# Kernel tuning notes

Measured on AMD Instinct MI355X. Metric: run time of the kernel, lower is better.

The kernel has to match this reference:

```python
import jax, jax.numpy as jnp
import numpy as np

B, T, IN, H, C = 256, 128, 64, 512, 11


def setup_inputs() -> dict:
    key = jax.random.key(0)
    ks = jax.random.split(key, 10)
    sc = 1.0 / np.sqrt(H).astype(np.float32)
    def w(k, shape, s):
        return jax.random.normal(k, shape, dtype=jnp.float32) * s
    return {
        "x": jax.random.normal(ks[0], (B, T, IN), dtype=jnp.float32),
        "t": jax.random.uniform(ks[1], (B, T), dtype=jnp.float32),
        # nn.LSTMCell params (gate order i, f, g, o)
        "W_ih": w(ks[2], (4 * H, IN), sc),
        "W_hh": w(ks[3], (4 * H, H), sc),
        "b_ih": jnp.zeros((4 * H,), jnp.float32),
        "b_hh": jnp.zeros((4 * H,), jnp.float32),
        # f_node: Linear(H,H) -> Tanh -> Linear(H,H)
        "W1": w(ks[4], (H, H), sc),
        "b1": jnp.zeros((H,), jnp.float32),
        "W2": w(ks[5], (H, H), sc),
        "b2": jnp.zeros((H,), jnp.float32),
        # ODELSTM per-step output Linear(H, out_feature=H)
        "Wo": w(ks[6], (H, H), sc),
        "bo": jnp.zeros((H,), jnp.float32),
        # model head Linear(H, num_classes)
        "Wc": w(ks[7], (C, H), sc),
        "bc": jnp.zeros((C,), jnp.float32),
    }


def reference(x, t, W_ih, W_hh, b_ih, b_hh, W1, b1, W2, b2, Wo, bo, Wc, bc):
    def f_node(y):  # [B,H] -> [B,H]
        return jnp.tanh(y @ W1.T + b1) @ W2.T + b2

    def rk4(y, dt):  # dt: [B,1]
        k1 = f_node(y)
        k2 = f_node(y + k1 * dt * 0.5)
        k3 = f_node(y + k2 * dt * 0.5)
        k4 = f_node(y + k3 * dt)
        return y + dt * (k1 + 2.0 * k2 + 2.0 * k3 + k4) / 6.0

    def step(carry, inp):
        h, c = carry
        xt, ts = inp  # [B,IN], [B]
        z = xt @ W_ih.T + h @ W_hh.T + (b_ih + b_hh)
        i, f, g, o = jnp.split(z, 4, axis=-1)
        c = jax.nn.sigmoid(f) * c + jax.nn.sigmoid(i) * jnp.tanh(g)
        h = jax.nn.sigmoid(o) * jnp.tanh(c)
        dt = (ts * (1.0 / 3.0))[:, None]  # 3 fixed unfolds per timestep
        for _ in range(3):
            h = rk4(h, dt)
        out = h @ Wo.T + bo  # ODELSTM per-step output projection
        return (h, c), out

    h0 = jnp.zeros((x.shape[0], W_hh.shape[1]), x.dtype)
    (_h, _c), outs = jax.lax.scan(
        step, (h0, h0), (jnp.swapaxes(x, 0, 1), jnp.swapaxes(t, 0, 1))
    )
    outs = jnp.swapaxes(outs, 0, 1)  # [B,T,H]
    return outs @ Wc.T + bc  # [B,T,num_classes]
```

## Files before the change

kernel.cpp:

```cpp
#include <hip/hip_runtime.h>
#include <stdint.h>


#define H_  512
#define B_  256
#define T_  128
#define IN_ 64
#define NC_ 11
#define LD_ 520
#define FSTRIDE 64

typedef _Float16 h8v __attribute__((ext_vector_type(8)));
typedef float    f4v __attribute__((ext_vector_type(4)));
typedef unsigned long long ull;

__device__ __forceinline__ float fsigm(float x) { return 1.0f / (1.0f + __expf(-x)); }
__device__ __forceinline__ float ftanh(float x) { return 1.0f - 2.0f / (1.0f + __expf(2.0f * x)); }


__global__ void prep_M(const float* __restrict__ W1, const float* __restrict__ W2,
                       float* __restrict__ Mtmp) {
  __shared__ float w1s[8][512];
  int tid = threadIdx.x;
  int n0 = blockIdx.x * 8;
  for (int i = tid; i < 8 * 512; i += 256) {
    int nn = i >> 9, m = i & 511;
    w1s[nn][m] = W1[(n0 + nn) * 512 + m];
  }
  __syncthreads();
  float acc0[8] = {0,0,0,0,0,0,0,0}, acc1[8] = {0,0,0,0,0,0,0,0};
  for (int m = 0; m < 512; ++m) {
    float a = W2[m * 512 + tid];
    float b = W2[m * 512 + 256 + tid];
#pragma unroll
    for (int j = 0; j < 8; ++j) { acc0[j] += a * w1s[j][m]; acc1[j] += b * w1s[j][m]; }
  }
  for (int j = 0; j < 8; ++j) {
    Mtmp[(size_t)tid * 512 + n0 + j]         = acc0[j];
    Mtmp[(size_t)(tid + 256) * 512 + n0 + j] = acc1[j];
  }
}

__global__ void prep_small(const float* __restrict__ W1, const float* __restrict__ b2,
                           const float* __restrict__ Wc, const float* __restrict__ Wo,
                           const float* __restrict__ bo, const float* __restrict__ bc,
                           float* __restrict__ dvec, float* __restrict__ Wco,
                           float* __restrict__ bprime) {
  __shared__ float wcs[NC_ * 512];
  int tid = threadIdx.x;
  if (blockIdx.x == 0) {
    for (int n = tid; n < 512; n += 256) {
      float acc = 0.f;
      for (int m = 0; m < 512; ++m) acc += b2[m] * W1[n * 512 + m];
      dvec[n] = acc;
    }
  } else if (blockIdx.x == 1) {
    if (tid < NC_) {
      float acc = bc[tid];
      for (int m = 0; m < 512; ++m) acc += Wc[tid * 512 + m] * bo[m];
      bprime[tid] = acc;
    }
  } else {
    for (int i = tid; i < NC_ * 512; i += 256) wcs[i] = Wc[i];
    __syncthreads();
    int h = (blockIdx.x - 2) * 256 + tid;
    float acc[NC_];
#pragma unroll
    for (int c = 0; c < NC_; ++c) acc[c] = 0.f;
    for (int m = 0; m < 512; ++m) {
      float wo = Wo[m * 512 + h];
#pragma unroll
      for (int c = 0; c < NC_; ++c) acc[c] += wo * wcs[c * 512 + m];
    }
    for (int c = 0; c < NC_; ++c) Wco[c * 512 + h] = acc[c];
  }
}

__global__ void prep_wtilde(const float* __restrict__ Whh, const float* __restrict__ Wih,
                            _Float16* __restrict__ Wtil) {
  int gidx = blockIdx.x * 256 + threadIdx.x;
  int lane = gidx & 63, fb = gidx >> 6;
  int kc = fb % 18; int t2 = fb / 18;
  int t = t2 & 31, g = t2 >> 5;
  int n = g * 512 + t * 16 + (lane & 15);
  int k = kc * 32 + ((lane >> 4) & 3) * 8;
  _Float16 vals[8];
  if (k < 512) {
#pragma unroll
    for (int j = 0; j < 8; ++j) vals[j] = (_Float16)Whh[(size_t)n * 512 + k + j];
  } else {
#pragma unroll
    for (int j = 0; j < 8; ++j) vals[j] = (_Float16)Wih[(size_t)n * 64 + (k - 512) + j];
  }
  *(h8v*)(Wtil + (size_t)fb * 512 + lane * 8) = *(h8v*)vals;
}

__global__ void prep_fragW(const float* __restrict__ W, _Float16* __restrict__ dst) {
  int gidx = blockIdx.x * 256 + threadIdx.x;
  int lane = gidx & 63, fb = gidx >> 6;
  int t = fb >> 4, kc = fb & 15;
  int n = t * 16 + (lane & 15);
  int k = kc * 32 + ((lane >> 4) & 3) * 8;
  _Float16 vals[8];
#pragma unroll
  for (int j = 0; j < 8; ++j) vals[j] = (_Float16)W[(size_t)n * 512 + k + j];
  *(h8v*)(dst + (size_t)fb * 512 + lane * 8) = *(h8v*)vals;
}

__global__ void prep_fragM(const float* __restrict__ Mtmp, _Float16* __restrict__ dst) {
  int gidx = blockIdx.x * 256 + threadIdx.x;
  int lane = gidx & 63, fb = gidx >> 6;
  int t = fb >> 4, kc = fb & 15;
  int n = t * 16 + (lane & 15);
  int k = kc * 32 + ((lane >> 4) & 3) * 8;
  _Float16 vals[8];
#pragma unroll
  for (int j = 0; j < 8; ++j) vals[j] = (_Float16)Mtmp[(size_t)(k + j) * 512 + n];
  *(h8v*)(dst + (size_t)fb * 512 + lane * 8) = *(h8v*)vals;
}


__device__ __forceinline__ void phase_exchange(int* __restrict__ flagsC,
                                               ull* __restrict__ Xb,
                                               _Float16* __restrict__ ACT,
                                               int s, int phase) {
  const int tid = threadIdx.x;
  __syncthreads();
  {
    int m = tid >> 4, ch = tid & 15;
    ull v = *(const ull*)(ACT + m * LD_ + s * 64 + ch * 4);
    __hip_atomic_store(Xb + m * 128 + s * 16 + ch, v,
                       __ATOMIC_RELAXED, __HIP_MEMORY_SCOPE_AGENT);
  }
  __builtin_amdgcn_s_waitcnt(0);
  __syncthreads();
  if (tid == 0)
    __hip_atomic_store(flagsC + s * FSTRIDE, phase,
                       __ATOMIC_RELAXED, __HIP_MEMORY_SCOPE_AGENT);
  {
    const int* fp = flagsC + (tid & 7) * FSTRIDE;
    for (;;) {
      int f = __hip_atomic_load(fp, __ATOMIC_RELAXED, __HIP_MEMORY_SCOPE_AGENT);
      if (__all(f >= phase)) break;
      __builtin_amdgcn_s_sleep(1);
    }
  }
  __asm__ volatile("" ::: "memory");
  ull tv[8];
#pragma unroll
  for (int i = 0; i < 8; ++i) {
    int idx = i * 256 + tid;
    int os = idx >> 8, r = idx & 255, m = r >> 4, ch = r & 15;
    tv[i] = __hip_atomic_load(Xb + m * 128 + os * 16 + ch,
                              __ATOMIC_RELAXED, __HIP_MEMORY_SCOPE_AGENT);
  }
#pragma unroll
  for (int i = 0; i < 8; ++i) {
    int idx = i * 256 + tid;
    int os = idx >> 8, r = idx & 255, m = r >> 4, ch = r & 15;
    *(ull*)(ACT + m * LD_ + os * 64 + ch * 4) = tv[i];
  }
  __syncthreads();
}


__device__ __forceinline__ f4v mm_lds(const _Float16* __restrict__ ACT,
                                      const _Float16* __restrict__ Ws,
                                      int w, int lane) {
  f4v e = {0,0,0,0}, o = {0,0,0,0};
  const _Float16* arow = ACT + (lane & 15) * LD_ + (lane >> 4) * 8;
  const h8v* b = (const h8v*)Ws;
#pragma unroll
  for (int kc = 0; kc < 16; kc += 2) {
    e = __builtin_amdgcn_mfma_f32_16x16x32_f16(*(const h8v*)(arow + kc * 32),
                                               b[(w * 16 + kc) * 64 + lane], e, 0, 0, 0);
    o = __builtin_amdgcn_mfma_f32_16x16x32_f16(*(const h8v*)(arow + (kc + 1) * 32),
                                               b[(w * 16 + kc + 1) * 64 + lane], o, 0, 0, 0);
  }
  return e + o;
}

__device__ __forceinline__ f4v mm_reg(const _Float16* __restrict__ ACT,
                                      const h8v* __restrict__ mreg, int lane) {
  f4v e = {0,0,0,0}, o = {0,0,0,0};
  const _Float16* arow = ACT + (lane & 15) * LD_ + (lane >> 4) * 8;
#pragma unroll
  for (int kc = 0; kc < 16; kc += 2) {
    e = __builtin_amdgcn_mfma_f32_16x16x32_f16(*(const h8v*)(arow + kc * 32),
                                               mreg[kc], e, 0, 0, 0);
    o = __builtin_amdgcn_mfma_f32_16x16x32_f16(*(const h8v*)(arow + (kc + 1) * 32),
                                               mreg[kc + 1], o, 0, 0, 0);
  }
  return e + o;
}


__launch_bounds__(256, 1)
__global__ void recur(const float* __restrict__ x,
                      const float* __restrict__ tin,
                      const float* __restrict__ bih,
                      const float* __restrict__ bhh,
                      const float* __restrict__ b1g,
                      const float* __restrict__ b2g,
                      const _Float16* __restrict__ Wtil,
                      const _Float16* __restrict__ W1T,
                      const _Float16* __restrict__ W2T,
                      const _Float16* __restrict__ MF,
                      const float* __restrict__ dvec,
                      _Float16* __restrict__ Hsave,
                      ull* __restrict__ Xchg,
                      int* __restrict__ flags) {
  const int blk = blockIdx.x, c = blk & 15, s = blk >> 4;
  const int tid = threadIdx.x, w = tid >> 6, lane = tid & 63;
  const int lm = lane & 15, quad = lane >> 4;
  const int col = s * 64 + w * 16 + lm;

  __shared__ __align__(16) _Float16 W1s[4 * 16 * 512];
  __shared__ __align__(16) _Float16 W2s[4 * 16 * 512];
  __shared__ __align__(16) _Float16 ACT[16 * LD_];

  {
    const h8v* g1 = (const h8v*)(W1T + (size_t)s * 32768);
    const h8v* g2 = (const h8v*)(W2T + (size_t)s * 32768);
    h8v* l1 = (h8v*)W1s; h8v* l2 = (h8v*)W2s;
    for (int i = tid; i < 4096; i += 256) { l1[i] = g1[i]; l2[i] = g2[i]; }
  }
  h8v mreg[16];
  {
    const h8v* gm = (const h8v*)(MF + ((size_t)(4 * s + w) * 16) * 512);
#pragma unroll
    for (int kc = 0; kc < 16; ++kc) mreg[kc] = gm[kc * 64 + lane];
  }
  for (int i = tid; i < 16 * LD_; i += 256) ACT[i] = (_Float16)0.f;

  const float zb0 = bih[col] + bhh[col];
  const float zb1 = bih[512 + col] + bhh[512 + col];
  const float zb2 = bih[1024 + col] + bhh[1024 + col];
  const float zb3 = bih[1536 + col] + bhh[1536 + col];
  const float b1r = b1g[col], dvr = dvec[col], b2r = b2g[col];

  float c_[4] = {0,0,0,0}, h_[4] = {0,0,0,0};
  float u1a[4], SSa[4], SMa[4];
  int phase = 0;
  int* flagsC = flags + c * 512;
  __syncthreads();

  for (int ts = 0; ts < T_; ++ts) {
    float dt_[4];
#pragma unroll
    for (int r = 0; r < 4; ++r)
      dt_[r] = tin[(c * 16 + quad * 4 + r) * T_ + ts] * (1.0f / 3.0f);

    {
      f4v z0 = {0,0,0,0}, z1 = {0,0,0,0}, z2 = {0,0,0,0}, z3 = {0,0,0,0};
      const _Float16* arow = ACT + lm * LD_ + quad * 8;
      const h8v* wt = (const h8v*)Wtil;
      const int tb = 4 * s + w;
#pragma unroll
      for (int kc = 0; kc < 16; ++kc) {
        h8v av = *(const h8v*)(arow + kc * 32);
        z0 = __builtin_amdgcn_mfma_f32_16x16x32_f16(av, wt[(size_t)((0 * 32 + tb) * 18 + kc) * 64 + lane], z0, 0, 0, 0);
        z1 = __builtin_amdgcn_mfma_f32_16x16x32_f16(av, wt[(size_t)((1 * 32 + tb) * 18 + kc) * 64 + lane], z1, 0, 0, 0);
        z2 = __builtin_amdgcn_mfma_f32_16x16x32_f16(av, wt[(size_t)((2 * 32 + tb) * 18 + kc) * 64 + lane], z2, 0, 0, 0);
        z3 = __builtin_amdgcn_mfma_f32_16x16x32_f16(av, wt[(size_t)((3 * 32 + tb) * 18 + kc) * 64 + lane], z3, 0, 0, 0);
      }
      const float* xr = x + ((size_t)(c * 16 + lm) * T_ + ts) * IN_ + quad * 8;
#pragma unroll
      for (int kx = 0; kx < 2; ++kx) {
        float4 f0 = *(const float4*)(xr + kx * 32);
        float4 f1 = *(const float4*)(xr + kx * 32 + 4);
        h8v av;
        av[0] = (_Float16)f0.x; av[1] = (_Float16)f0.y; av[2] = (_Float16)f0.z; av[3] = (_Float16)f0.w;
        av[4] = (_Float16)f1.x; av[5] = (_Float16)f1.y; av[6] = (_Float16)f1.z; av[7] = (_Float16)f1.w;
        int kc = 16 + kx;
        z0 = __builtin_amdgcn_mfma_f32_16x16x32_f16(av, wt[(size_t)((0 * 32 + tb) * 18 + kc) * 64 + lane], z0, 0, 0, 0);
        z1 = __builtin_amdgcn_mfma_f32_16x16x32_f16(av, wt[(size_t)((1 * 32 + tb) * 18 + kc) * 64 + lane], z1, 0, 0, 0);
        z2 = __builtin_amdgcn_mfma_f32_16x16x32_f16(av, wt[(size_t)((2 * 32 + tb) * 18 + kc) * 64 + lane], z2, 0, 0, 0);
        z3 = __builtin_amdgcn_mfma_f32_16x16x32_f16(av, wt[(size_t)((3 * 32 + tb) * 18 + kc) * 64 + lane], z3, 0, 0, 0);
      }
      __syncthreads();
#pragma unroll
      for (int r = 0; r < 4; ++r) {
        float zi = z0[r] + zb0, zf = z1[r] + zb1, zg = z2[r] + zb2, zo = z3[r] + zb3;
        float cv = fsigm(zf) * c_[r] + fsigm(zi) * ftanh(zg);
        c_[r] = cv;
        h_[r] = fsigm(zo) * ftanh(cv);
        ACT[(quad * 4 + r) * LD_ + col] = (_Float16)h_[r];
      }
    }
    ++phase;
    phase_exchange(flagsC, Xchg + (size_t)((phase & 1) * 16 + c) * 2048, ACT, s, phase);

    {
      f4v D = mm_lds(ACT, W1s, w, lane);
      __syncthreads();
#pragma unroll
      for (int r = 0; r < 4; ++r) {
        float uv = D[r] + b1r;
        u1a[r] = uv;
        float t1v = ftanh(uv);
        SSa[r] = t1v;
        ACT[(quad * 4 + r) * LD_ + col] = (_Float16)t1v;
      }
    }
    ++phase;
    phase_exchange(flagsC, Xchg + (size_t)((phase & 1) * 16 + c) * 2048, ACT, s, phase);

#pragma unroll 1
    for (int uf = 0; uf < 3; ++uf) {
      {
        f4v D = mm_reg(ACT, mreg, lane);
        __syncthreads();
#pragma unroll
        for (int r = 0; r < 4; ++r) {
          float Dv = D[r];
          float u2 = u1a[r] + 0.5f * dt_[r] * (Dv + dvr);
          SMa[r] = Dv;
          float t2v = ftanh(u2);
          SSa[r] += 2.0f * t2v;
          ACT[(quad * 4 + r) * LD_ + col] = (_Float16)t2v;
        }
      }
      ++phase;
      phase_exchange(flagsC, Xchg + (size_t)((phase & 1) * 16 + c) * 2048, ACT, s, phase);

      {
        f4v D = mm_reg(ACT, mreg, lane);
        __syncthreads();
#pragma unroll
        for (int r = 0; r < 4; ++r) {
          float Dv = D[r];
          float u3 = u1a[r] + 0.5f * dt_[r] * (Dv + dvr);
          SMa[r] += 2.0f * Dv;
          float t3v = ftanh(u3);
          SSa[r] += 2.0f * t3v;
          ACT[(quad * 4 + r) * LD_ + col] = (_Float16)t3v;
        }
      }
      ++phase;
      phase_exchange(flagsC, Xchg + (size_t)((phase & 1) * 16 + c) * 2048, ACT, s, phase);

      {
        f4v D = mm_reg(ACT, mreg, lane);
        __syncthreads();
#pragma unroll
        for (int r = 0; r < 4; ++r) {
          float Dv = D[r];
          float u4 = u1a[r] + dt_[r] * (Dv + dvr);
          SMa[r] += 2.0f * Dv;
          float t4v = ftanh(u4);
          SSa[r] += t4v;
          ACT[(quad * 4 + r) * LD_ + col] = (uf < 2) ? (_Float16)t4v : (_Float16)SSa[r];
        }
      }
      ++phase;
      phase_exchange(flagsC, Xchg + (size_t)((phase & 1) * 16 + c) * 2048, ACT, s, phase);

      if (uf < 2) {
        f4v D = mm_reg(ACT, mreg, lane);
        __syncthreads();
#pragma unroll
        for (int r = 0; r < 4; ++r) {
          float Dv = D[r];
          SMa[r] += Dv;
          float un = u1a[r] + (dt_[r] * (1.0f / 6.0f)) * SMa[r] + dt_[r] * dvr;
          u1a[r] = un;
          float t1v = ftanh(un);
          SSa[r] += t1v;
          ACT[(quad * 4 + r) * LD_ + col] = (_Float16)t1v;
        }
        ++phase;
        phase_exchange(flagsC, Xchg + (size_t)((phase & 1) * 16 + c) * 2048, ACT, s, phase);
      }
    }

    {
      f4v D = mm_lds(ACT, W2s, w, lane);
      __syncthreads();
#pragma unroll
      for (int r = 0; r < 4; ++r) {
        h_[r] += (dt_[r] * (1.0f / 6.0f)) * D[r] + (3.0f * dt_[r]) * b2r;
        _Float16 hv = (_Float16)h_[r];
        ACT[(quad * 4 + r) * LD_ + col] = hv;
        Hsave[((size_t)(ts + 1) * B_ + c * 16 + quad * 4 + r) * H_ + col] = hv;
      }
    }
    ++phase;
    phase_exchange(flagsC, Xchg + (size_t)((phase & 1) * 16 + c) * 2048, ACT, s, phase);
  }
}

__global__ void final_out(const _Float16* __restrict__ Hsave,
                          const float* __restrict__ Wco,
                          const float* __restrict__ bprime,
                          float* __restrict__ out) {
  __shared__ float wcs[NC_][520];
  int tid = threadIdx.x;
  for (int i = tid; i < NC_ * 512; i += 256) wcs[i >> 9][i & 511] = Wco[i];
  __syncthreads();
  int r0 = blockIdx.x * 64;
  int rl = tid >> 4, cc = tid & 15;
  for (int pass = 0; pass < 4; ++pass) {
    int row = r0 + pass * 16 + rl;
    int b = row >> 7, t = row & 127;
    const _Float16* hrow = Hsave + ((size_t)(t + 1) * B_ + b) * H_;
    if (cc < NC_) {
      float acc = 0.f;
      for (int k8 = 0; k8 < 64; ++k8) {
        h8v hv = *(const h8v*)(hrow + k8 * 8);
#pragma unroll
        for (int j = 0; j < 8; ++j) acc += (float)hv[j] * wcs[cc][k8 * 8 + j];
      }
      out[(size_t)row * NC_ + cc] = acc + bprime[cc];
    }
  }
}

extern "C" void kernel_launch(void* const* d_in, const int* in_sizes, int n_in,
                              void* d_out, int out_size, void* d_ws, size_t ws_size,
                              hipStream_t stream) {
  (void)in_sizes; (void)n_in; (void)out_size; (void)ws_size;
  const float* x   = (const float*)d_in[0];
  const float* tin = (const float*)d_in[1];
  const float* Wih = (const float*)d_in[2];
  const float* Whh = (const float*)d_in[3];
  const float* bih = (const float*)d_in[4];
  const float* bhh = (const float*)d_in[5];
  const float* W1  = (const float*)d_in[6];
  const float* b1  = (const float*)d_in[7];
  const float* W2  = (const float*)d_in[8];
  const float* b2  = (const float*)d_in[9];
  const float* Wo  = (const float*)d_in[10];
  const float* bo  = (const float*)d_in[11];
  const float* Wc  = (const float*)d_in[12];
  const float* bc  = (const float*)d_in[13];

  char* ws = (char*)d_ws;
  size_t off = 0;
  auto alloc = [&](size_t bytes) -> void* {
    void* p = ws + off;
    off = (off + bytes + 1023) & ~(size_t)1023;
    return p;
  };
  _Float16* Wtil  = (_Float16*)alloc((size_t)2304 * 512 * 2);
  _Float16* W1T   = (_Float16*)alloc((size_t)512 * 512 * 2);
  _Float16* W2T   = (_Float16*)alloc((size_t)512 * 512 * 2);
  _Float16* MF    = (_Float16*)alloc((size_t)512 * 512 * 2);
  float*    Mtmp  = (float*)alloc((size_t)512 * 512 * 4);
  float*    dvec  = (float*)alloc(512 * 4);
  float*    WcoF  = (float*)alloc((size_t)NC_ * 512 * 4);
  float*    bprim = (float*)alloc(64);
  _Float16* Hsave = (_Float16*)alloc((size_t)(T_ + 1) * B_ * H_ * 2);
  ull*      Xchg  = (ull*)alloc((size_t)2 * 16 * 2048 * 8);
  int*      flags = (int*)alloc(16 * 512 * 4);

  hipMemsetAsync(flags, 0, 16 * 512 * 4, stream);

  prep_M<<<64, 256, 0, stream>>>(W1, W2, Mtmp);
  prep_small<<<4, 256, 0, stream>>>(W1, b2, Wc, Wo, bo, bc, dvec, WcoF, bprim);
  prep_wtilde<<<576, 256, 0, stream>>>(Whh, Wih, Wtil);
  prep_fragW<<<128, 256, 0, stream>>>(W1, W1T);
  prep_fragW<<<128, 256, 0, stream>>>(W2, W2T);
  prep_fragM<<<128, 256, 0, stream>>>(Mtmp, MF);
  recur<<<128, 256, 0, stream>>>(x, tin, bih, bhh, b1, b2, Wtil, W1T, W2T, MF,
                                 dvec, Hsave, Xchg, flags);
  final_out<<<512, 256, 0, stream>>>(Hsave, WcoF, bprim, (float*)d_out);
}
```

Measured before the change: 4.645 ms.

## Publish activations per-wave directly and use per-wave flags in phase exchange

Each wave now writes its four fp16 results straight from registers to the global exchange buffer in a column-major layout and raises its own per-wave flag, instead of staging through LDS and synchronizing the whole block twice before one thread sets a per-block flag. Readers poll 32 per-wave flags and scatter the gathered data back into the row-major LDS activation tile with transposing stores. This removes two block barriers and an LDS round-trip per phase. In exchange there is more flag polling traffic and strided 2-byte LDS stores that may bank-conflict.

```diff
diff --git a/kernel.cpp b/kernel.cpp
--- a/kernel.cpp
+++ b/kernel.cpp
@@ -11,6 +11,7 @@
 #define FSTRIDE 64
 
 typedef _Float16 h8v __attribute__((ext_vector_type(8)));
+typedef _Float16 h4v __attribute__((ext_vector_type(4)));
 typedef float    f4v __attribute__((ext_vector_type(4)));
 typedef unsigned long long ull;
 
@@ -121,24 +122,16 @@
 
 
 __device__ __forceinline__ void phase_exchange(int* __restrict__ flagsC,
-                                               ull* __restrict__ Xb,
+                                               const ull* __restrict__ Xb,
                                                _Float16* __restrict__ ACT,
-                                               int s, int phase) {
+                                               int s, int w, int lane, int phase) {
   const int tid = threadIdx.x;
-  __syncthreads();
-  {
-    int m = tid >> 4, ch = tid & 15;
-    ull v = *(const ull*)(ACT + m * LD_ + s * 64 + ch * 4);
-    __hip_atomic_store(Xb + m * 128 + s * 16 + ch, v,
-                       __ATOMIC_RELAXED, __HIP_MEMORY_SCOPE_AGENT);
-  }
   __builtin_amdgcn_s_waitcnt(0);
-  __syncthreads();
-  if (tid == 0)
-    __hip_atomic_store(flagsC + s * FSTRIDE, phase,
+  if (lane == 0)
+    __hip_atomic_store(flagsC + (s * 4 + w) * FSTRIDE, phase,
                        __ATOMIC_RELAXED, __HIP_MEMORY_SCOPE_AGENT);
   {
-    const int* fp = flagsC + (tid & 7) * FSTRIDE;
+    const int* fp = flagsC + (lane & 31) * FSTRIDE;
     for (;;) {
       int f = __hip_atomic_load(fp, __ATOMIC_RELAXED, __HIP_MEMORY_SCOPE_AGENT);
       if (__all(f >= phase)) break;
@@ -148,17 +141,17 @@
   __asm__ volatile("" ::: "memory");
   ull tv[8];
 #pragma unroll
-  for (int i = 0; i < 8; ++i) {
-    int idx = i * 256 + tid;
-    int os = idx >> 8, r = idx & 255, m = r >> 4, ch = r & 15;
-    tv[i] = __hip_atomic_load(Xb + m * 128 + os * 16 + ch,
-                              __ATOMIC_RELAXED, __HIP_MEMORY_SCOPE_AGENT);
-  }
-#pragma unroll
-  for (int i = 0; i < 8; ++i) {
-    int idx = i * 256 + tid;
-    int os = idx >> 8, r = idx & 255, m = r >> 4, ch = r & 15;
-    *(ull*)(ACT + m * LD_ + os * 64 + ch * 4) = tv[i];
+  for (int os = 0; os < 8; ++os)
+    tv[os] = __hip_atomic_load(Xb + os * 256 + tid,
+                               __ATOMIC_RELAXED, __HIP_MEMORY_SCOPE_AGENT);
+  {
+    const int colq = tid >> 2, q4 = (tid & 3) * 4;
+#pragma unroll
+    for (int os = 0; os < 8; ++os) {
+      h4v v = __builtin_bit_cast(h4v, tv[os]);
+      _Float16* dst = ACT + q4 * LD_ + os * 64 + colq;
+      dst[0] = v[0]; dst[LD_] = v[1]; dst[2 * LD_] = v[2]; dst[3 * LD_] = v[3];
+    }
   }
   __syncthreads();
 }
@@ -242,8 +235,12 @@
   float c_[4] = {0,0,0,0}, h_[4] = {0,0,0,0};
   float u1a[4], SSa[4], SMa[4];
   int phase = 0;
-  int* flagsC = flags + c * 512;
+  int* flagsC = flags + c * 32 * FSTRIDE;
+  const size_t pubi = (size_t)col * 4 + quad;
   __syncthreads();
+
+#define PUBLISH(pv) __hip_atomic_store(Xb + pubi, __builtin_bit_cast(ull, pv), \
+                                       __ATOMIC_RELAXED, __HIP_MEMORY_SCOPE_AGENT)
 
   for (int ts = 0; ts < T_; ++ts) {
     float dt_[4];
@@ -278,39 +275,45 @@
         z2 = __builtin_amdgcn_mfma_f32_16x16x32_f16(av, wt[(size_t)((2 * 32 + tb) * 18 + kc) * 64 + lane], z2, 0, 0, 0);
         z3 = __builtin_amdgcn_mfma_f32_16x16x32_f16(av, wt[(size_t)((3 * 32 + tb) * 18 + kc) * 64 + lane], z3, 0, 0, 0);
       }
-      __syncthreads();
+      ++phase;
+      ull* Xb = Xchg + (size_t)((phase & 1) * 16 + c) * 2048;
+      h4v pv;
 #pragma unroll
       for (int r = 0; r < 4; ++r) {
         float zi = z0[r] + zb0, zf = z1[r] + zb1, zg = z2[r] + zb2, zo = z3[r] + zb3;
         float cv = fsigm(zf) * c_[r] + fsigm(zi) * ftanh(zg);
         c_[r] = cv;
         h_[r] = fsigm(zo) * ftanh(cv);
-        ACT[(quad * 4 + r) * LD_ + col] = (_Float16)h_[r];
-      }
-    }
-    ++phase;
-    phase_exchange(flagsC, Xchg + (size_t)((phase & 1) * 16 + c) * 2048, ACT, s, phase);
+        pv[r] = (_Float16)h_[r];
+      }
+      PUBLISH(pv);
+      phase_exchange(flagsC, Xb, ACT, s, w, lane, phase);
+    }
 
     {
       f4v D = mm_lds(ACT, W1s, w, lane);
-      __syncthreads();
+      ++phase;
+      ull* Xb = Xchg + (size_t)((phase & 1) * 16 + c) * 2048;
+      h4v pv;
 #pragma unroll
       for (int r = 0; r < 4; ++r) {
         float uv = D[r] + b1r;
         u1a[r] = uv;
         float t1v = ftanh(uv);
         SSa[r] = t1v;
-        ACT[(quad * 4 + r) * LD_ + col] = (_Float16)t1v;
-      }
-    }
-    ++phase;
-    phase_exchange(flagsC, Xchg + (size_t)((phase & 1) * 16 + c) * 2048, ACT, s, phase);
+        pv[r] = (_Float16)t1v;
+      }
+      PUBLISH(pv);
+      phase_exchange(flagsC, Xb, ACT, s, w, lane, phase);
+    }
 
 #pragma unroll 1
     for (int uf = 0; uf < 3; ++uf) {
       {
         f4v D = mm_reg(ACT, mreg, lane);
-        __syncthreads();
+        ++phase;
+        ull* Xb = Xchg + (size_t)((phase & 1) * 16 + c) * 2048;
+        h4v pv;
 #pragma unroll
         for (int r = 0; r < 4; ++r) {
           float Dv = D[r];
@@ -318,15 +321,17 @@
           SMa[r] = Dv;
           float t2v = ftanh(u2);
           SSa[r] += 2.0f * t2v;
-          ACT[(quad * 4 + r) * LD_ + col] = (_Float16)t2v;
+          pv[r] = (_Float16)t2v;
         }
-      }
-      ++phase;
-      phase_exchange(flagsC, Xchg + (size_t)((phase & 1) * 16 + c) * 2048, ACT, s, phase);
+        PUBLISH(pv);
+        phase_exchange(flagsC, Xb, ACT, s, w, lane, phase);
+      }
 
       {
         f4v D = mm_reg(ACT, mreg, lane);
-        __syncthreads();
+        ++phase;
+        ull* Xb = Xchg + (size_t)((phase & 1) * 16 + c) * 2048;
+        h4v pv;
 #pragma unroll
         for (int r = 0; r < 4; ++r) {
           float Dv = D[r];
@@ -334,15 +339,17 @@
           SMa[r] += 2.0f * Dv;
           float t3v = ftanh(u3);
           SSa[r] += 2.0f * t3v;
-          ACT[(quad * 4 + r) * LD_ + col] = (_Float16)t3v;
+          pv[r] = (_Float16)t3v;
         }
-      }
-      ++phase;
-      phase_exchange(flagsC, Xchg + (size_t)((phase & 1) * 16 + c) * 2048, ACT, s, phase);
+        PUBLISH(pv);
+        phase_exchange(flagsC, Xb, ACT, s, w, lane, phase);
+      }
 
       {
         f4v D = mm_reg(ACT, mreg, lane);
-        __syncthreads();
+        ++phase;
+        ull* Xb = Xchg + (size_t)((phase & 1) * 16 + c) * 2048;
+        h4v pv;
 #pragma unroll
         for (int r = 0; r < 4; ++r) {
           float Dv = D[r];
@@ -350,15 +357,17 @@
           SMa[r] += 2.0f * Dv;
           float t4v = ftanh(u4);
           SSa[r] += t4v;
-          ACT[(quad * 4 + r) * LD_ + col] = (uf < 2) ? (_Float16)t4v : (_Float16)SSa[r];
+          pv[r] = (uf < 2) ? (_Float16)t4v : (_Float16)SSa[r];
         }
-      }
-      ++phase;
-      phase_exchange(flagsC, Xchg + (size_t)((phase & 1) * 16 + c) * 2048, ACT, s, phase);
+        PUBLISH(pv);
+        phase_exchange(flagsC, Xb, ACT, s, w, lane, phase);
+      }
 
       if (uf < 2) {
         f4v D = mm_reg(ACT, mreg, lane);
-        __syncthreads();
+        ++phase;
+        ull* Xb = Xchg + (size_t)((phase & 1) * 16 + c) * 2048;
+        h4v pv;
 #pragma unroll
         for (int r = 0; r < 4; ++r) {
           float Dv = D[r];
@@ -367,27 +376,30 @@
           u1a[r] = un;
           float t1v = ftanh(un);
           SSa[r] += t1v;
-          ACT[(quad * 4 + r) * LD_ + col] = (_Float16)t1v;
+          pv[r] = (_Float16)t1v;
         }
-        ++phase;
-        phase_exchange(flagsC, Xchg + (size_t)((phase & 1) * 16 + c) * 2048, ACT, s, phase);
+        PUBLISH(pv);
+        phase_exchange(flagsC, Xb, ACT, s, w, lane, phase);
       }
     }
 
     {
       f4v D = mm_lds(ACT, W2s, w, lane);
-      __syncthreads();
+      ++phase;
+      ull* Xb = Xchg + (size_t)((phase & 1) * 16 + c) * 2048;
+      h4v pv;
 #pragma unroll
       for (int r = 0; r < 4; ++r) {
         h_[r] += (dt_[r] * (1.0f / 6.0f)) * D[r] + (3.0f * dt_[r]) * b2r;
         _Float16 hv = (_Float16)h_[r];
-        ACT[(quad * 4 + r) * LD_ + col] = hv;
+        pv[r] = hv;
         Hsave[((size_t)(ts + 1) * B_ + c * 16 + quad * 4 + r) * H_ + col] = hv;
       }
-    }
-    ++phase;
-    phase_exchange(flagsC, Xchg + (size_t)((phase & 1) * 16 + c) * 2048, ACT, s, phase);
-  }
+      PUBLISH(pv);
+      phase_exchange(flagsC, Xb, ACT, s, w, lane, phase);
+    }
+  }
+#undef PUBLISH
 }
 
 __global__ void final_out(const _Float16* __restrict__ Hsave,
@@ -452,9 +464,9 @@
   float*    bprim = (float*)alloc(64);
   _Float16* Hsave = (_Float16*)alloc((size_t)(T_ + 1) * B_ * H_ * 2);
   ull*      Xchg  = (ull*)alloc((size_t)2 * 16 * 2048 * 8);
-  int*      flags = (int*)alloc(16 * 512 * 4);
-
-  hipMemsetAsync(flags, 0, 16 * 512 * 4, stream);
+  int*      flags = (int*)alloc(16 * 32 * FSTRIDE * 4);
+
+  hipMemsetAsync(flags, 0, 16 * 32 * FSTRIDE * 4, stream);
 
   prep_M<<<64, 256, 0, stream>>>(W1, W2, Mtmp);
   prep_small<<<4, 256, 0, stream>>>(W1, b2, Wc, Wo, bo, bc, dvec, WcoF, bprim);
```

After: 5.920 ms. 27.5% more time.

## Replace flag-based block barrier with epoch-tagged data exchange

Applied to the files above, without the earlier changes.

Each exchanged value now carries its phase number in the upper 32 bits of a 64-bit word. Consumers poll the data slots directly until every tag reaches the current phase, which removes the separate flag stores, the waitcnt, and two of the __syncthreads per exchange, and threads publish straight from registers instead of staging through LDS. The cost is that each exchanged word holds half as much fp16 payload, so exchange traffic doubles, and every thread spins on several remote loads.

```diff
diff --git a/kernel.cpp b/kernel.cpp
--- a/kernel.cpp
+++ b/kernel.cpp
@@ -8,11 +8,11 @@
 #define IN_ 64
 #define NC_ 11
 #define LD_ 520
-#define FSTRIDE 64
 
 typedef _Float16 h8v __attribute__((ext_vector_type(8)));
 typedef float    f4v __attribute__((ext_vector_type(4)));
 typedef unsigned long long ull;
+typedef unsigned int uint;
 
 __device__ __forceinline__ float fsigm(float x) { return 1.0f / (1.0f + __expf(-x)); }
 __device__ __forceinline__ float ftanh(float x) { return 1.0f - 2.0f / (1.0f + __expf(2.0f * x)); }
@@ -120,47 +120,66 @@
 }
 
 
-__device__ __forceinline__ void phase_exchange(int* __restrict__ flagsC,
-                                               ull* __restrict__ Xb,
+__device__ __forceinline__ ull pack2(_Float16 d0, _Float16 d1, int ep) {
+  uint lo = (uint)__builtin_bit_cast(unsigned short, d0) |
+            ((uint)__builtin_bit_cast(unsigned short, d1) << 16);
+  return (ull)lo | ((ull)(uint)ep << 32);
+}
+
+__device__ __forceinline__ void publish2(ull* __restrict__ XbA, ull* __restrict__ XbB,
+                                         int slot, const float* pv, int phase) {
+  ull eA = pack2((_Float16)pv[0], (_Float16)pv[1], phase);
+  ull eB = pack2((_Float16)pv[2], (_Float16)pv[3], phase);
+  __hip_atomic_store(XbA + slot, eA, __ATOMIC_RELAXED, __HIP_MEMORY_SCOPE_AGENT);
+  __hip_atomic_store(XbB + slot, eB, __ATOMIC_RELAXED, __HIP_MEMORY_SCOPE_AGENT);
+}
+
+__device__ __forceinline__ void store_tile(_Float16* __restrict__ ACT, int q, int cg,
+                                           const ull* a, const ull* b) {
+  uint l0 = (uint)a[0], l1 = (uint)a[1], l2 = (uint)a[2], l3 = (uint)a[3];
+  uint m0 = (uint)b[0], m1 = (uint)b[1], m2 = (uint)b[2], m3 = (uint)b[3];
+  ull r0 = (ull)((l0 & 0xffffu) | (l1 << 16)) | ((ull)((l2 & 0xffffu) | (l3 << 16)) << 32);
+  ull r1 = (ull)((l0 >> 16) | (l1 & 0xffff0000u)) | ((ull)((l2 >> 16) | (l3 & 0xffff0000u)) << 32);
+  ull r2 = (ull)((m0 & 0xffffu) | (m1 << 16)) | ((ull)((m2 & 0xffffu) | (m3 << 16)) << 32);
+  ull r3 = (ull)((m0 >> 16) | (m1 & 0xffff0000u)) | ((ull)((m2 >> 16) | (m3 & 0xffff0000u)) << 32);
+  _Float16* dst = ACT + (q * 4) * LD_ + cg * 4;
+  *(ull*)(dst)           = r0;
+  *(ull*)(dst + LD_)     = r1;
+  *(ull*)(dst + 2 * LD_) = r2;
+  *(ull*)(dst + 3 * LD_) = r3;
+}
+
+__device__ __forceinline__ void gather_restage(const ull* __restrict__ XbA,
+                                               const ull* __restrict__ XbB,
                                                _Float16* __restrict__ ACT,
-                                               int s, int phase) {
+                                               int s, int lane, int phase) {
   const int tid = threadIdx.x;
-  __syncthreads();
-  {
-    int m = tid >> 4, ch = tid & 15;
-    ull v = *(const ull*)(ACT + m * LD_ + s * 64 + ch * 4);
-    __hip_atomic_store(Xb + m * 128 + s * 16 + ch, v,
-                       __ATOMIC_RELAXED, __HIP_MEMORY_SCOPE_AGENT);
-  }
-  __builtin_amdgcn_s_waitcnt(0);
-  __syncthreads();
-  if (tid == 0)
-    __hip_atomic_store(flagsC + s * FSTRIDE, phase,
-                       __ATOMIC_RELAXED, __HIP_MEMORY_SCOPE_AGENT);
-  {
-    const int* fp = flagsC + (tid & 7) * FSTRIDE;
-    for (;;) {
-      int f = __hip_atomic_load(fp, __ATOMIC_RELAXED, __HIP_MEMORY_SCOPE_AGENT);
-      if (__all(f >= phase)) break;
-      __builtin_amdgcn_s_sleep(1);
-    }
-  }
-  __asm__ volatile("" ::: "memory");
-  ull tv[8];
-#pragma unroll
-  for (int i = 0; i < 8; ++i) {
-    int idx = i * 256 + tid;
-    int os = idx >> 8, r = idx & 255, m = r >> 4, ch = r & 15;
-    tv[i] = __hip_atomic_load(Xb + m * 128 + os * 16 + ch,
-                              __ATOMIC_RELAXED, __HIP_MEMORY_SCOPE_AGENT);
-  }
-#pragma unroll
-  for (int i = 0; i < 8; ++i) {
-    int idx = i * 256 + tid;
-    int os = idx >> 8, r = idx & 255, m = r >> 4, ch = r & 15;
-    *(ull*)(ACT + m * LD_ + os * 64 + ch * 4) = tv[i];
-  }
-  __syncthreads();
+  const int q0 = tid >> 7, cg = tid & 127;
+  const int base0 = q0 * 512 + cg * 4;
+  const int base1 = (q0 + 2) * 512 + cg * 4;
+  const int gslot = s * 64 + (lane & 3) * 16;
+  const uint p = (uint)phase;
+  ull a0[4], b0[4], a1[4], b1[4];
+  for (;;) {
+    ull g = __hip_atomic_load(XbA + gslot, __ATOMIC_RELAXED, __HIP_MEMORY_SCOPE_AGENT);
+#pragma unroll
+    for (int j = 0; j < 4; ++j) {
+      a0[j] = __hip_atomic_load(XbA + base0 + j, __ATOMIC_RELAXED, __HIP_MEMORY_SCOPE_AGENT);
+      b0[j] = __hip_atomic_load(XbB + base0 + j, __ATOMIC_RELAXED, __HIP_MEMORY_SCOPE_AGENT);
+      a1[j] = __hip_atomic_load(XbA + base1 + j, __ATOMIC_RELAXED, __HIP_MEMORY_SCOPE_AGENT);
+      b1[j] = __hip_atomic_load(XbB + base1 + j, __ATOMIC_RELAXED, __HIP_MEMORY_SCOPE_AGENT);
+    }
+    bool ok = ((uint)(g >> 32) >= p);
+#pragma unroll
+    for (int j = 0; j < 4; ++j) {
+      ok = ok && ((uint)(a0[j] >> 32) >= p) && ((uint)(b0[j] >> 32) >= p) &&
+                 ((uint)(a1[j] >> 32) >= p) && ((uint)(b1[j] >> 32) >= p);
+    }
+    if (__all(ok)) break;
+    __builtin_amdgcn_s_sleep(1);
+  }
+  store_tile(ACT, q0, cg, a0, b0);
+  store_tile(ACT, q0 + 2, cg, a1, b1);
 }
 
 
@@ -208,8 +227,7 @@
                       const _Float16* __restrict__ MF,
                       const float* __restrict__ dvec,
                       _Float16* __restrict__ Hsave,
-                      ull* __restrict__ Xchg,
-                      int* __restrict__ flags) {
+                      ull* __restrict__ Xchg) {
   const int blk = blockIdx.x, c = blk & 15, s = blk >> 4;
   const int tid = threadIdx.x, w = tid >> 6, lane = tid & 63;
   const int lm = lane & 15, quad = lane >> 4;
@@ -242,8 +260,11 @@
   float c_[4] = {0,0,0,0}, h_[4] = {0,0,0,0};
   float u1a[4], SSa[4], SMa[4];
   int phase = 0;
-  int* flagsC = flags + c * 512;
+  const int slotq = quad * 512 + col;
   __syncthreads();
+
+#define XSEL() ull* XbA = Xchg + (size_t)(((phase & 1) * 16 + c) * 2) * 2048; \
+               ull* XbB = XbA + 2048
 
   for (int ts = 0; ts < T_; ++ts) {
     float dt_[4];
@@ -278,39 +299,47 @@
         z2 = __builtin_amdgcn_mfma_f32_16x16x32_f16(av, wt[(size_t)((2 * 32 + tb) * 18 + kc) * 64 + lane], z2, 0, 0, 0);
         z3 = __builtin_amdgcn_mfma_f32_16x16x32_f16(av, wt[(size_t)((3 * 32 + tb) * 18 + kc) * 64 + lane], z3, 0, 0, 0);
       }
-      __syncthreads();
+      ++phase;
+      XSEL();
+      float pv[4];
 #pragma unroll
       for (int r = 0; r < 4; ++r) {
         float zi = z0[r] + zb0, zf = z1[r] + zb1, zg = z2[r] + zb2, zo = z3[r] + zb3;
         float cv = fsigm(zf) * c_[r] + fsigm(zi) * ftanh(zg);
         c_[r] = cv;
         h_[r] = fsigm(zo) * ftanh(cv);
-        ACT[(quad * 4 + r) * LD_ + col] = (_Float16)h_[r];
-      }
-    }
-    ++phase;
-    phase_exchange(flagsC, Xchg + (size_t)((phase & 1) * 16 + c) * 2048, ACT, s, phase);
+        pv[r] = h_[r];
+      }
+      publish2(XbA, XbB, slotq, pv, phase);
+      gather_restage(XbA, XbB, ACT, s, lane, phase);
+      __syncthreads();
+    }
 
     {
       f4v D = mm_lds(ACT, W1s, w, lane);
-      __syncthreads();
+      ++phase;
+      XSEL();
+      float pv[4];
 #pragma unroll
       for (int r = 0; r < 4; ++r) {
         float uv = D[r] + b1r;
         u1a[r] = uv;
         float t1v = ftanh(uv);
         SSa[r] = t1v;
-        ACT[(quad * 4 + r) * LD_ + col] = (_Float16)t1v;
-      }
-    }
-    ++phase;
-    phase_exchange(flagsC, Xchg + (size_t)((phase & 1) * 16 + c) * 2048, ACT, s, phase);
+        pv[r] = t1v;
+      }
+      publish2(XbA, XbB, slotq, pv, phase);
+      gather_restage(XbA, XbB, ACT, s, lane, phase);
+      __syncthreads();
+    }
 
 #pragma unroll 1
     for (int uf = 0; uf < 3; ++uf) {
       {
         f4v D = mm_reg(ACT, mreg, lane);
-        __syncthreads();
+        ++phase;
+        XSEL();
+        float pv[4];
 #pragma unroll
         for (int r = 0; r < 4; ++r) {
           float Dv = D[r];
@@ -318,15 +347,18 @@
           SMa[r] = Dv;
           float t2v = ftanh(u2);
           SSa[r] += 2.0f * t2v;
-          ACT[(quad * 4 + r) * LD_ + col] = (_Float16)t2v;
+          pv[r] = t2v;
         }
-      }
-      ++phase;
-      phase_exchange(flagsC, Xchg + (size_t)((phase & 1) * 16 + c) * 2048, ACT, s, phase);
+        publish2(XbA, XbB, slotq, pv, phase);
+        gather_restage(XbA, XbB, ACT, s, lane, phase);
+        __syncthreads();
+      }
 
       {
         f4v D = mm_reg(ACT, mreg, lane);
-        __syncthreads();
+        ++phase;
+        XSEL();
+        float pv[4];
 #pragma unroll
         for (int r = 0; r < 4; ++r) {
           float Dv = D[r];
@@ -334,15 +366,18 @@
           SMa[r] += 2.0f * Dv;
           float t3v = ftanh(u3);
           SSa[r] += 2.0f * t3v;
-          ACT[(quad * 4 + r) * LD_ + col] = (_Float16)t3v;
+          pv[r] = t3v;
         }
-      }
-      ++phase;
-      phase_exchange(flagsC, Xchg + (size_t)((phase & 1) * 16 + c) * 2048, ACT, s, phase);
+        publish2(XbA, XbB, slotq, pv, phase);
+        gather_restage(XbA, XbB, ACT, s, lane, phase);
+        __syncthreads();
+      }
 
       {
         f4v D = mm_reg(ACT, mreg, lane);
-        __syncthreads();
+        ++phase;
+        XSEL();
+        float pv[4];
 #pragma unroll
         for (int r = 0; r < 4; ++r) {
           float Dv = D[r];
@@ -350,15 +385,18 @@
           SMa[r] += 2.0f * Dv;
           float t4v = ftanh(u4);
           SSa[r] += t4v;
-          ACT[(quad * 4 + r) * LD_ + col] = (uf < 2) ? (_Float16)t4v : (_Float16)SSa[r];
+          pv[r] = (uf < 2) ? t4v : SSa[r];
         }
-      }
-      ++phase;
-      phase_exchange(flagsC, Xchg + (size_t)((phase & 1) * 16 + c) * 2048, ACT, s, phase);
+        publish2(XbA, XbB, slotq, pv, phase);
+        gather_restage(XbA, XbB, ACT, s, lane, phase);
+        __syncthreads();
+      }
 
       if (uf < 2) {
         f4v D = mm_reg(ACT, mreg, lane);
-        __syncthreads();
+        ++phase;
+        XSEL();
+        float pv[4];
 #pragma unroll
         for (int r = 0; r < 4; ++r) {
           float Dv = D[r];
@@ -367,27 +405,31 @@
           u1a[r] = un;
           float t1v = ftanh(un);
           SSa[r] += t1v;
-          ACT[(quad * 4 + r) * LD_ + col] = (_Float16)t1v;
+          pv[r] = t1v;
         }
-        ++phase;
-        phase_exchange(flagsC, Xchg + (size_t)((phase & 1) * 16 + c) * 2048, ACT, s, phase);
+        publish2(XbA, XbB, slotq, pv, phase);
+        gather_restage(XbA, XbB, ACT, s, lane, phase);
+        __syncthreads();
       }
     }
 
     {
       f4v D = mm_lds(ACT, W2s, w, lane);
-      __syncthreads();
+      ++phase;
+      XSEL();
+      float pv[4];
 #pragma unroll
       for (int r = 0; r < 4; ++r) {
         h_[r] += (dt_[r] * (1.0f / 6.0f)) * D[r] + (3.0f * dt_[r]) * b2r;
-        _Float16 hv = (_Float16)h_[r];
-        ACT[(quad * 4 + r) * LD_ + col] = hv;
-        Hsave[((size_t)(ts + 1) * B_ + c * 16 + quad * 4 + r) * H_ + col] = hv;
-      }
-    }
-    ++phase;
-    phase_exchange(flagsC, Xchg + (size_t)((phase & 1) * 16 + c) * 2048, ACT, s, phase);
-  }
+        pv[r] = h_[r];
+        Hsave[((size_t)(ts + 1) * B_ + c * 16 + quad * 4 + r) * H_ + col] = (_Float16)h_[r];
+      }
+      publish2(XbA, XbB, slotq, pv, phase);
+      gather_restage(XbA, XbB, ACT, s, lane, phase);
+      __syncthreads();
+    }
+  }
+#undef XSEL
 }
 
 __global__ void final_out(const _Float16* __restrict__ Hsave,
@@ -451,10 +493,9 @@
   float*    WcoF  = (float*)alloc((size_t)NC_ * 512 * 4);
   float*    bprim = (float*)alloc(64);
   _Float16* Hsave = (_Float16*)alloc((size_t)(T_ + 1) * B_ * H_ * 2);
-  ull*      Xchg  = (ull*)alloc((size_t)2 * 16 * 2048 * 8);
-  int*      flags = (int*)alloc(16 * 512 * 4);
-
-  hipMemsetAsync(flags, 0, 16 * 512 * 4, stream);
+  ull*      Xchg  = (ull*)alloc((size_t)2 * 16 * 2 * 2048 * 8);
+
+  hipMemsetAsync(Xchg, 0, (size_t)2 * 16 * 2 * 2048 * 8, stream);
 
   prep_M<<<64, 256, 0, stream>>>(W1, W2, Mtmp);
   prep_small<<<4, 256, 0, stream>>>(W1, b2, Wc, Wo, bo, bc, dvec, WcoF, bprim);
@@ -463,6 +504,6 @@
   prep_fragW<<<128, 256, 0, stream>>>(W2, W2T);
   prep_fragM<<<128, 256, 0, stream>>>(Mtmp, MF);
   recur<<<128, 256, 0, stream>>>(x, tin, bih, bhh, b1, b2, Wtil, W1T, W2T, MF,
-                                 dvec, Hsave, Xchg, flags);
+                                 dvec, Hsave, Xchg);
   final_out<<<512, 256, 0, stream>>>(Hsave, WcoF, bprim, (float*)d_out);
 }
```

Result: slower. 5.961 ms (+28.3%).

## Publish through a separate LDS buffer and use per-wave exchange flags

Applied to the files above, without the earlier changes.

Each phase now writes its new activations into a small dedicated LDS publish buffer instead of the shared ACT tile. This removes the block barrier that had to wait for all waves to finish their matmul reads of ACT before anyone could write to it. Readiness flags now live at wave granularity: each wave signals after its own global stores drain, which removes the second block barrier inside the exchange. The cost is that every wave polls 32 flags instead of 8, and the flag array is larger.

```diff
diff --git a/kernel.cpp b/kernel.cpp
--- a/kernel.cpp
+++ b/kernel.cpp
@@ -123,22 +123,22 @@
 __device__ __forceinline__ void phase_exchange(int* __restrict__ flagsC,
                                                ull* __restrict__ Xb,
                                                _Float16* __restrict__ ACT,
-                                               int s, int phase) {
+                                               const _Float16* __restrict__ PUB,
+                                               int s, int w, int lane, int phase) {
   const int tid = threadIdx.x;
   __syncthreads();
   {
     int m = tid >> 4, ch = tid & 15;
-    ull v = *(const ull*)(ACT + m * LD_ + s * 64 + ch * 4);
+    ull v = *(const ull*)(PUB + m * 64 + ch * 4);
     __hip_atomic_store(Xb + m * 128 + s * 16 + ch, v,
                        __ATOMIC_RELAXED, __HIP_MEMORY_SCOPE_AGENT);
   }
   __builtin_amdgcn_s_waitcnt(0);
-  __syncthreads();
-  if (tid == 0)
-    __hip_atomic_store(flagsC + s * FSTRIDE, phase,
+  if (lane == 0)
+    __hip_atomic_store(flagsC + (s * 4 + w) * FSTRIDE, phase,
                        __ATOMIC_RELAXED, __HIP_MEMORY_SCOPE_AGENT);
   {
-    const int* fp = flagsC + (tid & 7) * FSTRIDE;
+    const int* fp = flagsC + (lane & 31) * FSTRIDE;
     for (;;) {
       int f = __hip_atomic_load(fp, __ATOMIC_RELAXED, __HIP_MEMORY_SCOPE_AGENT);
       if (__all(f >= phase)) break;
@@ -218,6 +218,7 @@
   __shared__ __align__(16) _Float16 W1s[4 * 16 * 512];
   __shared__ __align__(16) _Float16 W2s[4 * 16 * 512];
   __shared__ __align__(16) _Float16 ACT[16 * LD_];
+  __shared__ __align__(16) _Float16 PUB[16 * 64];
 
   {
     const h8v* g1 = (const h8v*)(W1T + (size_t)s * 32768);
@@ -242,7 +243,8 @@
   float c_[4] = {0,0,0,0}, h_[4] = {0,0,0,0};
   float u1a[4], SSa[4], SMa[4];
   int phase = 0;
-  int* flagsC = flags + c * 512;
+  int* flagsC = flags + c * 32 * FSTRIDE;
+  const int pub0 = w * 16 + lm;
   __syncthreads();
 
   for (int ts = 0; ts < T_; ++ts) {
@@ -278,39 +280,40 @@
         z2 = __builtin_amdgcn_mfma_f32_16x16x32_f16(av, wt[(size_t)((2 * 32 + tb) * 18 + kc) * 64 + lane], z2, 0, 0, 0);
         z3 = __builtin_amdgcn_mfma_f32_16x16x32_f16(av, wt[(size_t)((3 * 32 + tb) * 18 + kc) * 64 + lane], z3, 0, 0, 0);
       }
-      __syncthreads();
+      ++phase;
+      ull* Xb = Xchg + (size_t)((phase & 1) * 16 + c) * 2048;
 #pragma unroll
       for (int r = 0; r < 4; ++r) {
         float zi = z0[r] + zb0, zf = z1[r] + zb1, zg = z2[r] + zb2, zo = z3[r] + zb3;
         float cv = fsigm(zf) * c_[r] + fsigm(zi) * ftanh(zg);
         c_[r] = cv;
         h_[r] = fsigm(zo) * ftanh(cv);
-        ACT[(quad * 4 + r) * LD_ + col] = (_Float16)h_[r];
-      }
-    }
-    ++phase;
-    phase_exchange(flagsC, Xchg + (size_t)((phase & 1) * 16 + c) * 2048, ACT, s, phase);
+        PUB[(quad * 4 + r) * 64 + pub0] = (_Float16)h_[r];
+      }
+      phase_exchange(flagsC, Xb, ACT, PUB, s, w, lane, phase);
+    }
 
     {
       f4v D = mm_lds(ACT, W1s, w, lane);
-      __syncthreads();
+      ++phase;
+      ull* Xb = Xchg + (size_t)((phase & 1) * 16 + c) * 2048;
 #pragma unroll
       for (int r = 0; r < 4; ++r) {
         float uv = D[r] + b1r;
         u1a[r] = uv;
         float t1v = ftanh(uv);
         SSa[r] = t1v;
-        ACT[(quad * 4 + r) * LD_ + col] = (_Float16)t1v;
-      }
-    }
-    ++phase;
-    phase_exchange(flagsC, Xchg + (size_t)((phase & 1) * 16 + c) * 2048, ACT, s, phase);
+        PUB[(quad * 4 + r) * 64 + pub0] = (_Float16)t1v;
+      }
+      phase_exchange(flagsC, Xb, ACT, PUB, s, w, lane, phase);
+    }
 
 #pragma unroll 1
     for (int uf = 0; uf < 3; ++uf) {
       {
         f4v D = mm_reg(ACT, mreg, lane);
-        __syncthreads();
+        ++phase;
+        ull* Xb = Xchg + (size_t)((phase & 1) * 16 + c) * 2048;
 #pragma unroll
         for (int r = 0; r < 4; ++r) {
           float Dv = D[r];
@@ -318,15 +321,15 @@
           SMa[r] = Dv;
           float t2v = ftanh(u2);
           SSa[r] += 2.0f * t2v;
-          ACT[(quad * 4 + r) * LD_ + col] = (_Float16)t2v;
+          PUB[(quad * 4 + r) * 64 + pub0] = (_Float16)t2v;
         }
-      }
-      ++phase;
-      phase_exchange(flagsC, Xchg + (size_t)((phase & 1) * 16 + c) * 2048, ACT, s, phase);
+        phase_exchange(flagsC, Xb, ACT, PUB, s, w, lane, phase);
+      }
 
       {
         f4v D = mm_reg(ACT, mreg, lane);
-        __syncthreads();
+        ++phase;
+        ull* Xb = Xchg + (size_t)((phase & 1) * 16 + c) * 2048;
 #pragma unroll
         for (int r = 0; r < 4; ++r) {
           float Dv = D[r];
@@ -334,15 +337,15 @@
           SMa[r] += 2.0f * Dv;
           float t3v = ftanh(u3);
           SSa[r] += 2.0f * t3v;
-          ACT[(quad * 4 + r) * LD_ + col] = (_Float16)t3v;
+          PUB[(quad * 4 + r) * 64 + pub0] = (_Float16)t3v;
         }
-      }
-      ++phase;
-      phase_exchange(flagsC, Xchg + (size_t)((phase & 1) * 16 + c) * 2048, ACT, s, phase);
+        phase_exchange(flagsC, Xb, ACT, PUB, s, w, lane, phase);
+      }
 
       {
         f4v D = mm_reg(ACT, mreg, lane);
-        __syncthreads();
+        ++phase;
+        ull* Xb = Xchg + (size_t)((phase & 1) * 16 + c) * 2048;
 #pragma unroll
         for (int r = 0; r < 4; ++r) {
           float Dv = D[r];
@@ -350,15 +353,15 @@
           SMa[r] += 2.0f * Dv;
           float t4v = ftanh(u4);
           SSa[r] += t4v;
-          ACT[(quad * 4 + r) * LD_ + col] = (uf < 2) ? (_Float16)t4v : (_Float16)SSa[r];
+          PUB[(quad * 4 + r) * 64 + pub0] = (uf < 2) ? (_Float16)t4v : (_Float16)SSa[r];
         }
-      }
-      ++phase;
-      phase_exchange(flagsC, Xchg + (size_t)((phase & 1) * 16 + c) * 2048, ACT, s, phase);
+        phase_exchange(flagsC, Xb, ACT, PUB, s, w, lane, phase);
+      }
 
       if (uf < 2) {
         f4v D = mm_reg(ACT, mreg, lane);
-        __syncthreads();
+        ++phase;
+        ull* Xb = Xchg + (size_t)((phase & 1) * 16 + c) * 2048;
 #pragma unroll
         for (int r = 0; r < 4; ++r) {
           float Dv = D[r];
@@ -367,26 +370,25 @@
           u1a[r] = un;
           float t1v = ftanh(un);
           SSa[r] += t1v;
-          ACT[(quad * 4 + r) * LD_ + col] = (_Float16)t1v;
+          PUB[(quad * 4 + r) * 64 + pub0] = (_Float16)t1v;
         }
-        ++phase;
-        phase_exchange(flagsC, Xchg + (size_t)((phase & 1) * 16 + c) * 2048, ACT, s, phase);
+        phase_exchange(flagsC, Xb, ACT, PUB, s, w, lane, phase);
       }
     }
 
     {
       f4v D = mm_lds(ACT, W2s, w, lane);
-      __syncthreads();
+      ++phase;
+      ull* Xb = Xchg + (size_t)((phase & 1) * 16 + c) * 2048;
 #pragma unroll
       for (int r = 0; r < 4; ++r) {
         h_[r] += (dt_[r] * (1.0f / 6.0f)) * D[r] + (3.0f * dt_[r]) * b2r;
         _Float16 hv = (_Float16)h_[r];
-        ACT[(quad * 4 + r) * LD_ + col] = hv;
+        PUB[(quad * 4 + r) * 64 + pub0] = hv;
         Hsave[((size_t)(ts + 1) * B_ + c * 16 + quad * 4 + r) * H_ + col] = hv;
       }
-    }
-    ++phase;
-    phase_exchange(flagsC, Xchg + (size_t)((phase & 1) * 16 + c) * 2048, ACT, s, phase);
+      phase_exchange(flagsC, Xb, ACT, PUB, s, w, lane, phase);
+    }
   }
 }
 
@@ -452,9 +454,9 @@
   float*    bprim = (float*)alloc(64);
   _Float16* Hsave = (_Float16*)alloc((size_t)(T_ + 1) * B_ * H_ * 2);
   ull*      Xchg  = (ull*)alloc((size_t)2 * 16 * 2048 * 8);
-  int*      flags = (int*)alloc(16 * 512 * 4);
-
-  hipMemsetAsync(flags, 0, 16 * 512 * 4, stream);
+  int*      flags = (int*)alloc((size_t)16 * 32 * FSTRIDE * 4);
+
+  hipMemsetAsync(flags, 0, (size_t)16 * 32 * FSTRIDE * 4, stream);
 
   prep_M<<<64, 256, 0, stream>>>(W1, W2, Mtmp);
   prep_small<<<4, 256, 0, stream>>>(W1, b2, Wc, Wo, bo, bc, dvec, WcoF, bprim);
```

After: 5.938 ms. 1.28x slower.
